# Optimization experiments

Hardware: AMD Instinct MI355X
Metric: run time of the kernel (lower is better)

The kernel has to match this reference:

```python
import jax, jax.numpy as jnp
import numpy as np

N = 50000      # occupied sparse voxels
C_IN = 512     # inplanes (= 4*planes for residual)
P = 128        # planes
K = 27         # 3x3x3 kernel volume in 3D
EPS = 1e-5
NEG = 0.1      # leaky-relu slope


def setup_inputs() -> dict:
    key = jax.random.key(0)
    k1, k2, k3, k4, k5, k6 = jax.random.split(key, 6)
    x = jax.random.normal(k1, (N, C_IN), dtype=jnp.float32)
    mask = (jax.random.uniform(k2, (N, 1)) > 0.3).astype(jnp.float32)
    nbr = jax.random.randint(k3, (N, K), 0, N, dtype=jnp.int32)
    W1 = jax.random.normal(k4, (C_IN, P), dtype=jnp.float32) * (1.0 / np.sqrt(C_IN))
    W2 = jax.random.normal(k5, (K, P, P), dtype=jnp.float32) * (1.0 / np.sqrt(K * P))
    W3 = jax.random.normal(k6, (P, C_IN), dtype=jnp.float32) * (1.0 / np.sqrt(P))
    return {"x": x, "mask": mask, "nbr": nbr, "W1": W1, "W2": W2, "W3": W3}


def lrelu(x):
    return jnp.where(x >= 0, x, NEG * x)


def inorm(x):
    # Minkowski instance norm: per-channel over all points of the instance
    mu = jnp.mean(x, axis=0, keepdims=True)
    var = jnp.var(x, axis=0, keepdims=True)
    return (x - mu) * jax.lax.rsqrt(var + EPS)


def pconv_k1(x, m, W):
    # 1x1x1 partial conv: mask, matmul, renormalize by coverage (=m itself)
    valid = (m > 0).astype(x.dtype)          # [N,1]
    return (x @ W) * valid, valid


def pconv_k3(x, m, nbr, W):
    # gather-GEMM partial conv over 27-neighborhood map
    mg = m[nbr]                                # [N,K,1]
    xg = x[nbr] * mg                           # [N,K,P] masked gather
    out = jnp.einsum('nkc,kcd->nd', xg, W)     # [N,P]
    msum = jnp.sum(mg, axis=1)                 # [N,1] coverage count
    ratio = (K / jnp.maximum(msum, 1.0)) * (msum > 0).astype(x.dtype)
    return out * ratio, (msum > 0).astype(x.dtype)


def reference(x, mask, nbr, W1, W2, W3):
    out, m = pconv_k1(x, mask, W1)
    out = lrelu(inorm(out))
    out, m = pconv_k3(out, m, nbr, W2)
    out = lrelu(inorm(out))
    out, m = pconv_k1(out, m, W3)
    out = inorm(out)
    out = lrelu(out + x)                       # residual (no downsample)
    m = jnp.clip(m + mask, 0.0, 1.0)           # mask residual + clamp
    return out, m
```

## Files before the change

### kernel.cpp

```cpp
#include <hip/hip_runtime.h>
#include <hip/hip_bf16.h>

#define NPTS 50000
#define CIN  512
#define PCH  128
#define KNB  27
#define EPSV 1e-5f
#define NEGS 0.1f

typedef __bf16 bf16;
typedef __bf16 bf16x8 __attribute__((ext_vector_type(8)));
typedef __bf16 bf16x4 __attribute__((ext_vector_type(4)));
typedef float  f32x4  __attribute__((ext_vector_type(4)));

typedef void __attribute__((address_space(3)))* as3ptr;
typedef const void __attribute__((address_space(1)))* as1ptr;
__device__ __forceinline__ void gl_lds16(const void* g, void* l) {
  __builtin_amdgcn_global_load_lds((as1ptr)g, (as3ptr)l, 16, 0, 0);
}


__global__ void xcvt_kernel(const float* __restrict__ x, bf16* __restrict__ xb) {
  int i = (blockIdx.x * blockDim.x + threadIdx.x) * 8;
  if (i >= NPTS * CIN) return;
  float4 a = *(const float4*)&x[i];
  float4 b = *(const float4*)&x[i + 4];
  bf16x8 o;
  o[0] = (bf16)a.x; o[1] = (bf16)a.y; o[2] = (bf16)a.z; o[3] = (bf16)a.w;
  o[4] = (bf16)b.x; o[5] = (bf16)b.y; o[6] = (bf16)b.z; o[7] = (bf16)b.w;
  *(bf16x8*)&xb[i] = o;
}

__global__ void tcvt_kernel(const float* __restrict__ src, bf16* __restrict__ dst,
                            int R, int Ccols) {
  int i = blockIdx.x * blockDim.x + threadIdx.x;
  if (i >= R * Ccols) return;
  int c = i / R, r = i - c * R;
  dst[i] = (bf16)src[(size_t)r * Ccols + c];
}

__global__ void tcvt_w2k_kernel(const float* __restrict__ src, bf16* __restrict__ dst) {
  int i = blockIdx.x * blockDim.x + threadIdx.x;
  if (i >= KNB * PCH * PCH) return;
  int k = i >> 14, rem = i & 16383;
  int d = rem >> 7, c = rem & 127;
  dst[i] = (bf16)src[(k << 14) + c * 128 + d];
}

__global__ void prep_kernel(const int* __restrict__ nbr, const float* __restrict__ mask,
                            int* __restrict__ nbrT, float* __restrict__ ratio,
                            float* __restrict__ valid2) {
  int n = blockIdx.x * blockDim.x + threadIdx.x;
  if (n >= NPTS) return;
  float s = 0.f;
#pragma unroll
  for (int k = 0; k < KNB; ++k) {
    int idx = nbr[n * KNB + k];
    nbrT[k * NPTS + n] = idx;
    s += (mask[idx] > 0.f) ? 1.f : 0.f;
  }
  ratio[n]  = s > 0.f ? 27.0f / s : 0.f;
  valid2[n] = s > 0.f ? 1.f : 0.f;
}

__global__ void finalize_kernel(const float* __restrict__ ssum, const float* __restrict__ ssq,
                                float* __restrict__ mu, float* __restrict__ inv) {
  int c = threadIdx.x;
  float m = ssum[c] / (float)NPTS;
  float v = ssq[c] / (float)NPTS - m * m;
  mu[c]  = m;
  inv[c] = rsqrtf(v + EPSV);
}

__global__ void ew_kernel(const float* __restrict__ in, const float* __restrict__ mu,
                          const float* __restrict__ inv, const float* __restrict__ rowmask,
                          bf16* __restrict__ outb) {
  int i = (blockIdx.x * blockDim.x + threadIdx.x) * 4;
  if (i >= NPTS * PCH) return;
  float4 v = *(const float4*)&in[i];
  int c = i & 127;
  int row = i >> 7;
  float mk = rowmask[row];
  float t0 = (v.x - mu[c + 0]) * inv[c + 0];
  float t1 = (v.y - mu[c + 1]) * inv[c + 1];
  float t2 = (v.z - mu[c + 2]) * inv[c + 2];
  float t3 = (v.w - mu[c + 3]) * inv[c + 3];
  t0 = (t0 >= 0.f ? t0 : NEGS * t0) * mk;
  t1 = (t1 >= 0.f ? t1 : NEGS * t1) * mk;
  t2 = (t2 >= 0.f ? t2 : NEGS * t2) * mk;
  t3 = (t3 >= 0.f ? t3 : NEGS * t3) * mk;
  bf16x4 o;
  o[0] = (bf16)t0; o[1] = (bf16)t1; o[2] = (bf16)t2; o[3] = (bf16)t3;
  *(bf16x4*)&outb[i] = o;
}

__global__ void final_kernel(const float* __restrict__ x, const bf16* __restrict__ out3n,
                             const float* __restrict__ mu, const float* __restrict__ inv,
                             float* __restrict__ out) {
  int i = (blockIdx.x * blockDim.x + threadIdx.x) * 8;
  if (i >= NPTS * CIN) return;
  bf16x8 v = *(const bf16x8*)&out3n[i];
  float4 x0 = *(const float4*)&x[i];
  float4 x1 = *(const float4*)&x[i + 4];
  int c = i & 511;
  float t[8];
  float xv[8] = {x0.x, x0.y, x0.z, x0.w, x1.x, x1.y, x1.z, x1.w};
#pragma unroll
  for (int q = 0; q < 8; ++q) {
    float u = ((float)v[q] - mu[c + q]) * inv[c + q] + xv[q];
    t[q] = u >= 0.f ? u : NEGS * u;
  }
  float4 o0 = {t[0], t[1], t[2], t[3]}, o1 = {t[4], t[5], t[6], t[7]};
  *(float4*)&out[i] = o0;
  *(float4*)&out[i + 4] = o1;
}

__global__ void maskout_kernel(const float* __restrict__ mask, const float* __restrict__ valid2,
                               float* __restrict__ outm) {
  int n = blockIdx.x * blockDim.x + threadIdx.x;
  if (n >= NPTS) return;
  outm[n] = fminf(valid2[n] + mask[n], 1.f);
}


__global__ __launch_bounds__(256) void gemm1_kernel(
    const bf16* __restrict__ xb, const bf16* __restrict__ w1t,
    const float* __restrict__ mask, float* __restrict__ out1,
    float* __restrict__ ssum, float* __restrict__ ssq) {
  __shared__ __align__(16) bf16 As[2][128 * 128];
  int row0 = blockIdx.x * 128;
  int tid = threadIdx.x;
  int lane = tid & 63, wid = tid >> 6;
  int mq = (wid >> 1) * 64, nq = (wid & 1) * 64;
  int lr = lane & 15, lq = lane >> 4;
  int rb = tid >> 4;
  int msw = (tid & 15) ^ (rb & 7);
  int rowc[8];
#pragma unroll
  for (int j = 0; j < 8; ++j) {
    int rr = row0 + rb + 16 * j;
    rowc[j] = rr < NPTS ? rr : NPTS - 1;
  }
  f32x4 acc[4][4];
#pragma unroll
  for (int i = 0; i < 4; ++i)
#pragma unroll
    for (int j = 0; j < 4; ++j)
#pragma unroll
      for (int r = 0; r < 4; ++r) acc[i][j][r] = 0.f;

#pragma unroll
  for (int j = 0; j < 8; ++j)
    gl_lds16(xb + (size_t)rowc[j] * CIN + (msw << 3),
             &As[0][(j * 256 + wid * 64) * 8]);
  __syncthreads();

  for (int kc = 0; kc < 4; ++kc) {
    int cur = kc & 1;
    if (kc < 3) {
#pragma unroll
      for (int j = 0; j < 8; ++j)
        gl_lds16(xb + (size_t)rowc[j] * CIN + (kc + 1) * 128 + (msw << 3),
                 &As[cur ^ 1][(j * 256 + wid * 64) * 8]);
    }
    const bf16* bp = w1t + (size_t)(nq + lr) * CIN + kc * 128 + lq * 8;
#pragma unroll
    for (int c0 = 0; c0 < 128; c0 += 32) {
      int cs = ((c0 >> 3) + lq) ^ (lr & 7);
      bf16x8 af[4], bfg[4];
#pragma unroll
      for (int i = 0; i < 4; ++i) af[i]  = *(const bf16x8*)&As[cur][(mq + i * 16 + lr) * 128 + cs * 8];
#pragma unroll
      for (int i = 0; i < 4; ++i) bfg[i] = *(const bf16x8*)(bp + (size_t)i * 16 * CIN + c0);
#pragma unroll
      for (int i = 0; i < 4; ++i)
#pragma unroll
        for (int j = 0; j < 4; ++j)
          acc[i][j] = __builtin_amdgcn_mfma_f32_16x16x32_bf16(af[i], bfg[j], acc[i][j], 0, 0, 0);
    }
    __syncthreads();
  }
  float rs[4][4];
#pragma unroll
  for (int i = 0; i < 4; ++i)
#pragma unroll
    for (int r = 0; r < 4; ++r) {
      int row = row0 + mq + i * 16 + lq * 4 + r;
      rs[i][r] = (row < NPTS) ? (mask[row] > 0.f ? 1.f : 0.f) : 0.f;
    }
#pragma unroll
  for (int j = 0; j < 4; ++j) {
    int col = nq + j * 16 + lr;
    float s = 0.f, q = 0.f;
#pragma unroll
    for (int i = 0; i < 4; ++i) {
#pragma unroll
      for (int r = 0; r < 4; ++r) {
        int row = row0 + mq + i * 16 + lq * 4 + r;
        if (row < NPTS) {
          float v = acc[i][j][r] * rs[i][r];
          out1[(size_t)row * PCH + col] = v;
          s += v; q += v * v;
        }
      }
    }
    s += __shfl_xor(s, 16); s += __shfl_xor(s, 32);
    q += __shfl_xor(q, 16); q += __shfl_xor(q, 32);
    if (lq == 0) { atomicAdd(&ssum[col], s); atomicAdd(&ssq[col], q); }
  }
}

__global__ __launch_bounds__(256) void gemm2_kernel(
    const bf16* __restrict__ a, const bf16* __restrict__ w2k,
    const int* __restrict__ nbrT, const float* __restrict__ ratio,
    float* __restrict__ out2, float* __restrict__ ssum, float* __restrict__ ssq) {
  __shared__ __align__(16) bf16 As[2][128 * 128];
  int row0 = blockIdx.x * 128;
  int tid = threadIdx.x;
  int lane = tid & 63, wid = tid >> 6;
  int mq = (wid >> 1) * 64, nq = (wid & 1) * 64;
  int lr = lane & 15, lq = lane >> 4;
  int rb = tid >> 4;
  int msw = (tid & 15) ^ (rb & 7);
  int rowc[8];
#pragma unroll
  for (int j = 0; j < 8; ++j) {
    int rr = row0 + rb + 16 * j;
    rowc[j] = rr < NPTS ? rr : NPTS - 1;
  }
  f32x4 acc[4][4];
#pragma unroll
  for (int i = 0; i < 4; ++i)
#pragma unroll
    for (int j = 0; j < 4; ++j)
#pragma unroll
      for (int r = 0; r < 4; ++r) acc[i][j][r] = 0.f;

  int nidx[8];
#pragma unroll
  for (int j = 0; j < 8; ++j) nidx[j] = nbrT[rowc[j]];
#pragma unroll
  for (int j = 0; j < 8; ++j)
    gl_lds16(a + (size_t)nidx[j] * PCH + (msw << 3),
             &As[0][(j * 256 + wid * 64) * 8]);
#pragma unroll
  for (int j = 0; j < 8; ++j) nidx[j] = nbrT[NPTS + rowc[j]];
  __syncthreads();

  for (int k = 0; k < KNB; ++k) {
    int cur = k & 1;
    if (k + 1 < KNB) {
#pragma unroll
      for (int j = 0; j < 8; ++j)
        gl_lds16(a + (size_t)nidx[j] * PCH + (msw << 3),
                 &As[cur ^ 1][(j * 256 + wid * 64) * 8]);
    }
    if (k + 2 < KNB) {
#pragma unroll
      for (int j = 0; j < 8; ++j) nidx[j] = nbrT[(k + 2) * NPTS + rowc[j]];
    }
    const bf16* bp = w2k + (size_t)k * PCH * PCH + (nq + lr) * PCH + lq * 8;
#pragma unroll
    for (int c0 = 0; c0 < 128; c0 += 32) {
      int cs = ((c0 >> 3) + lq) ^ (lr & 7);
      bf16x8 af[4], bfg[4];
#pragma unroll
      for (int i = 0; i < 4; ++i) af[i]  = *(const bf16x8*)&As[cur][(mq + i * 16 + lr) * 128 + cs * 8];
#pragma unroll
      for (int i = 0; i < 4; ++i) bfg[i] = *(const bf16x8*)(bp + (size_t)i * 16 * PCH + c0);
#pragma unroll
      for (int i = 0; i < 4; ++i)
#pragma unroll
        for (int j = 0; j < 4; ++j)
          acc[i][j] = __builtin_amdgcn_mfma_f32_16x16x32_bf16(af[i], bfg[j], acc[i][j], 0, 0, 0);
    }
    __syncthreads();
  }
  float rs[4][4];
#pragma unroll
  for (int i = 0; i < 4; ++i)
#pragma unroll
    for (int r = 0; r < 4; ++r) {
      int row = row0 + mq + i * 16 + lq * 4 + r;
      rs[i][r] = (row < NPTS) ? ratio[row] : 0.f;
    }
#pragma unroll
  for (int j = 0; j < 4; ++j) {
    int col = nq + j * 16 + lr;
    float s = 0.f, q = 0.f;
#pragma unroll
    for (int i = 0; i < 4; ++i) {
#pragma unroll
      for (int r = 0; r < 4; ++r) {
        int row = row0 + mq + i * 16 + lq * 4 + r;
        if (row < NPTS) {
          float v = acc[i][j][r] * rs[i][r];
          out2[(size_t)row * PCH + col] = v;
          s += v; q += v * v;
        }
      }
    }
    s += __shfl_xor(s, 16); s += __shfl_xor(s, 32);
    q += __shfl_xor(q, 16); q += __shfl_xor(q, 32);
    if (lq == 0) { atomicAdd(&ssum[col], s); atomicAdd(&ssq[col], q); }
  }
}

__global__ __launch_bounds__(256) void gemm3_kernel(
    const bf16* __restrict__ a, const bf16* __restrict__ w3t, bf16* __restrict__ out3n,
    float* __restrict__ ssum, float* __restrict__ ssq) {
  __shared__ __align__(16) bf16 As[128 * 128];
  int row0 = blockIdx.x * 128;
  int ncol0 = blockIdx.y * 128;
  int tid = threadIdx.x;
  int lane = tid & 63, wid = tid >> 6;
  int mq = (wid >> 1) * 64, nq = (wid & 1) * 64;
  int lr = lane & 15, lq = lane >> 4;
  int rb = tid >> 4;
  int msw = (tid & 15) ^ (rb & 7);
#pragma unroll
  for (int j = 0; j < 8; ++j) {
    int rr = row0 + rb + 16 * j;
    int rc = rr < NPTS ? rr : NPTS - 1;
    gl_lds16(a + (size_t)rc * PCH + (msw << 3),
             &As[(j * 256 + wid * 64) * 8]);
  }
  f32x4 acc[4][4];
#pragma unroll
  for (int i = 0; i < 4; ++i)
#pragma unroll
    for (int j = 0; j < 4; ++j)
#pragma unroll
      for (int r = 0; r < 4; ++r) acc[i][j][r] = 0.f;
  __syncthreads();
  const bf16* bp = w3t + (size_t)(ncol0 + nq + lr) * PCH + lq * 8;
#pragma unroll
  for (int c0 = 0; c0 < 128; c0 += 32) {
    int cs = ((c0 >> 3) + lq) ^ (lr & 7);
    bf16x8 af[4], bfg[4];
#pragma unroll
    for (int i = 0; i < 4; ++i) af[i]  = *(const bf16x8*)&As[(mq + i * 16 + lr) * 128 + cs * 8];
#pragma unroll
    for (int i = 0; i < 4; ++i) bfg[i] = *(const bf16x8*)(bp + (size_t)i * 16 * PCH + c0);
#pragma unroll
    for (int i = 0; i < 4; ++i)
#pragma unroll
      for (int j = 0; j < 4; ++j)
        acc[i][j] = __builtin_amdgcn_mfma_f32_16x16x32_bf16(af[i], bfg[j], acc[i][j], 0, 0, 0);
  }
#pragma unroll
  for (int j = 0; j < 4; ++j) {
    int col = ncol0 + nq + j * 16 + lr;
    float s = 0.f, q = 0.f;
#pragma unroll
    for (int i = 0; i < 4; ++i) {
#pragma unroll
      for (int r = 0; r < 4; ++r) {
        int row = row0 + mq + i * 16 + lq * 4 + r;
        if (row < NPTS) {
          float v = acc[i][j][r];
          out3n[(size_t)row * CIN + col] = (bf16)v;
          s += v; q += v * v;
        }
      }
    }
    s += __shfl_xor(s, 16); s += __shfl_xor(s, 32);
    q += __shfl_xor(q, 16); q += __shfl_xor(q, 32);
    if (lq == 0) { atomicAdd(&ssum[col], s); atomicAdd(&ssq[col], q); }
  }
}

extern "C" void kernel_launch(void* const* d_in, const int* in_sizes, int n_in,
                              void* d_out, int out_size, void* d_ws, size_t ws_size,
                              hipStream_t stream) {
  const float* x    = (const float*)d_in[0];
  const float* mask = (const float*)d_in[1];
  const int*   nbr  = (const int*)d_in[2];
  const float* W1   = (const float*)d_in[3];
  const float* W2   = (const float*)d_in[4];
  const float* W3   = (const float*)d_in[5];
  float* out = (float*)d_out;
  char* ws = (char*)d_ws;

  auto al = [](size_t x_) { return (x_ + 255) & ~(size_t)255; };
  size_t off = 0;
  size_t OFF_OUT1  = off; off += al((size_t)NPTS * PCH * 4);
  size_t OFF_OUT2  = off; off += al((size_t)NPTS * PCH * 4);
  size_t OFF_OUT1N = off; off += al((size_t)NPTS * PCH * 2);
  size_t OFF_OUT2N = off; off += al((size_t)NPTS * PCH * 2);
  size_t OFF_W1T   = off; off += al((size_t)PCH * CIN * 2);
  size_t OFF_W2K   = off; off += al((size_t)KNB * PCH * PCH * 2);
  size_t OFF_W3T   = off; off += al((size_t)CIN * PCH * 2);
  size_t OFF_NBRT  = off; off += al((size_t)KNB * NPTS * 4);
  size_t OFF_RATIO = off; off += al((size_t)NPTS * 4);
  size_t OFF_VAL2  = off; off += al((size_t)NPTS * 4);
  size_t OFF_SUMS  = off; off += al((size_t)1536 * 4);
  size_t OFF_PRMS  = off; off += al((size_t)1536 * 4);

  float* out1   = (float*)(ws + OFF_OUT1);
  float* out2   = (float*)(ws + OFF_OUT2);
  bf16*  out3n  = (bf16*)(ws + OFF_OUT1);
  bf16*  xb     = (bf16*)(ws + OFF_OUT2);
  bf16*  out1n  = (bf16*)(ws + OFF_OUT1N);
  bf16*  out2n  = (bf16*)(ws + OFF_OUT2N);
  bf16*  w1t    = (bf16*)(ws + OFF_W1T);
  bf16*  w2k    = (bf16*)(ws + OFF_W2K);
  bf16*  w3t    = (bf16*)(ws + OFF_W3T);
  int*   nbrT   = (int*)(ws + OFF_NBRT);
  float* ratio  = (float*)(ws + OFF_RATIO);
  float* valid2 = (float*)(ws + OFF_VAL2);
  float* sums   = (float*)(ws + OFF_SUMS);
  float* s1sum = sums, *s1sq = sums + 128;
  float* s2sum = sums + 256, *s2sq = sums + 384;
  float* s3sum = sums + 512, *s3sq = sums + 1024;
  float* prms = (float*)(ws + OFF_PRMS);
  float* mu1 = prms, *inv1 = prms + 128;
  float* mu2 = prms + 256, *inv2 = prms + 384;
  float* mu3 = prms + 512, *inv3 = prms + 1024;

  hipMemsetAsync(sums, 0, 1536 * 4, stream);

  prep_kernel<<<(NPTS + 255) / 256, 256, 0, stream>>>(nbr, mask, nbrT, ratio, valid2);
  tcvt_kernel<<<(CIN * PCH + 255) / 256, 256, 0, stream>>>(W1, w1t, CIN, PCH);
  tcvt_w2k_kernel<<<(KNB * PCH * PCH + 255) / 256, 256, 0, stream>>>(W2, w2k);
  tcvt_kernel<<<(PCH * CIN + 255) / 256, 256, 0, stream>>>(W3, w3t, PCH, CIN);
  xcvt_kernel<<<(NPTS * CIN / 8 + 255) / 256, 256, 0, stream>>>(x, xb);

  int mblocks = (NPTS + 127) / 128;

  gemm1_kernel<<<mblocks, 256, 0, stream>>>(xb, w1t, mask, out1, s1sum, s1sq);
  finalize_kernel<<<1, 128, 0, stream>>>(s1sum, s1sq, mu1, inv1);
  ew_kernel<<<(NPTS * PCH / 4 + 255) / 256, 256, 0, stream>>>(out1, mu1, inv1, mask, out1n);

  gemm2_kernel<<<mblocks, 256, 0, stream>>>(out1n, w2k, nbrT, ratio, out2, s2sum, s2sq);
  finalize_kernel<<<1, 128, 0, stream>>>(s2sum, s2sq, mu2, inv2);
  ew_kernel<<<(NPTS * PCH / 4 + 255) / 256, 256, 0, stream>>>(out2, mu2, inv2, valid2, out2n);

  dim3 g3(mblocks, 4);
  gemm3_kernel<<<g3, 256, 0, stream>>>(out2n, w3t, out3n, s3sum, s3sq);
  finalize_kernel<<<1, 512, 0, stream>>>(s3sum, s3sq, mu3, inv3);
  final_kernel<<<(NPTS * CIN / 8 + 255) / 256, 256, 0, stream>>>(x, out3n, mu3, inv3, out);
  maskout_kernel<<<(NPTS + 255) / 256, 256, 0, stream>>>(mask, valid2, out + (size_t)NPTS * CIN);
}
```

Baseline: 505.7 us.

## Merge prep kernels, fold mask output into final, retile GEMM warps, loop gemm3 columns

Five preprocessing launches (x conversion, three weight transposes, neighbor prep) become one preproc kernel, and the mask-output kernel is folded into the final elementwise kernel, cutting launch overhead. All three GEMMs change warp tiling from 64x64 per warp to 128 rows x 32 columns per warp, so each warp reads every A row from LDS and fewer B fragments per step. gemm3 now loops over four 128-column chunks inside one block, reusing the staged A tile instead of launching a 4-wide grid. This lowers parallelism for gemm3 and increases LDS reads of A per warp.

```diff
diff --git a/kernel.cpp b/kernel.cpp
--- a/kernel.cpp
+++ b/kernel.cpp
@@ -20,47 +20,61 @@
 }
 
 
-__global__ void xcvt_kernel(const float* __restrict__ x, bf16* __restrict__ xb) {
-  int i = (blockIdx.x * blockDim.x + threadIdx.x) * 8;
-  if (i >= NPTS * CIN) return;
-  float4 a = *(const float4*)&x[i];
-  float4 b = *(const float4*)&x[i + 4];
-  bf16x8 o;
-  o[0] = (bf16)a.x; o[1] = (bf16)a.y; o[2] = (bf16)a.z; o[3] = (bf16)a.w;
-  o[4] = (bf16)b.x; o[5] = (bf16)b.y; o[6] = (bf16)b.z; o[7] = (bf16)b.w;
-  *(bf16x8*)&xb[i] = o;
-}
-
-__global__ void tcvt_kernel(const float* __restrict__ src, bf16* __restrict__ dst,
-                            int R, int Ccols) {
+__global__ void preproc_kernel(const float* __restrict__ x, const float* __restrict__ mask,
+                               const int* __restrict__ nbr,
+                               const float* __restrict__ W1, const float* __restrict__ W2,
+                               const float* __restrict__ W3,
+                               bf16* __restrict__ xb, int* __restrict__ nbrT,
+                               float* __restrict__ ratio, float* __restrict__ valid2,
+                               bf16* __restrict__ w1t, bf16* __restrict__ w2k,
+                               bf16* __restrict__ w3t) {
   int i = blockIdx.x * blockDim.x + threadIdx.x;
-  if (i >= R * Ccols) return;
-  int c = i / R, r = i - c * R;
-  dst[i] = (bf16)src[(size_t)r * Ccols + c];
-}
-
-__global__ void tcvt_w2k_kernel(const float* __restrict__ src, bf16* __restrict__ dst) {
-  int i = blockIdx.x * blockDim.x + threadIdx.x;
-  if (i >= KNB * PCH * PCH) return;
-  int k = i >> 14, rem = i & 16383;
-  int d = rem >> 7, c = rem & 127;
-  dst[i] = (bf16)src[(k << 14) + c * 128 + d];
-}
-
-__global__ void prep_kernel(const int* __restrict__ nbr, const float* __restrict__ mask,
-                            int* __restrict__ nbrT, float* __restrict__ ratio,
-                            float* __restrict__ valid2) {
-  int n = blockIdx.x * blockDim.x + threadIdx.x;
-  if (n >= NPTS) return;
-  float s = 0.f;
-#pragma unroll
-  for (int k = 0; k < KNB; ++k) {
-    int idx = nbr[n * KNB + k];
-    nbrT[k * NPTS + n] = idx;
-    s += (mask[idx] > 0.f) ? 1.f : 0.f;
-  }
-  ratio[n]  = s > 0.f ? 27.0f / s : 0.f;
-  valid2[n] = s > 0.f ? 1.f : 0.f;
+  const int NX = NPTS * CIN / 8;
+  if (i < NX) {
+    int e = i * 8;
+    float4 a = *(const float4*)&x[e];
+    float4 b = *(const float4*)&x[e + 4];
+    bf16x8 o;
+    o[0] = (bf16)a.x; o[1] = (bf16)a.y; o[2] = (bf16)a.z; o[3] = (bf16)a.w;
+    o[4] = (bf16)b.x; o[5] = (bf16)b.y; o[6] = (bf16)b.z; o[7] = (bf16)b.w;
+    *(bf16x8*)&xb[e] = o;
+    return;
+  }
+  i -= NX;
+  const int NW2 = KNB * PCH * PCH;
+  if (i < NW2) {
+    int k = i >> 14, rem = i & 16383;
+    int d = rem >> 7, c = rem & 127;
+    w2k[i] = (bf16)W2[(k << 14) + c * 128 + d];
+    return;
+  }
+  i -= NW2;
+  const int NW1 = CIN * PCH;
+  if (i < NW1) {
+    int c = i / CIN, r = i - c * CIN;
+    w1t[i] = (bf16)W1[r * PCH + c];
+    return;
+  }
+  i -= NW1;
+  const int NW3 = PCH * CIN;
+  if (i < NW3) {
+    int c = i / PCH, r = i - c * PCH;
+    w3t[i] = (bf16)W3[r * CIN + c];
+    return;
+  }
+  i -= NW3;
+  if (i < NPTS) {
+    int n = i;
+    float s = 0.f;
+#pragma unroll
+    for (int k = 0; k < KNB; ++k) {
+      int idx = nbr[n * KNB + k];
+      nbrT[k * NPTS + n] = idx;
+      s += (mask[idx] > 0.f) ? 1.f : 0.f;
+    }
+    ratio[n]  = s > 0.f ? 27.0f / s : 0.f;
+    valid2[n] = s > 0.f ? 1.f : 0.f;
+  }
 }
 
 __global__ void finalize_kernel(const float* __restrict__ ssum, const float* __restrict__ ssq,
@@ -96,8 +110,13 @@
 
 __global__ void final_kernel(const float* __restrict__ x, const bf16* __restrict__ out3n,
                              const float* __restrict__ mu, const float* __restrict__ inv,
+                             const float* __restrict__ mask, const float* __restrict__ valid2,
                              float* __restrict__ out) {
-  int i = (blockIdx.x * blockDim.x + threadIdx.x) * 8;
+  int gid = blockIdx.x * blockDim.x + threadIdx.x;
+  if (gid < NPTS) {
+    out[(size_t)NPTS * CIN + gid] = fminf(valid2[gid] + mask[gid], 1.f);
+  }
+  int i = gid * 8;
   if (i >= NPTS * CIN) return;
   bf16x8 v = *(const bf16x8*)&out3n[i];
   float4 x0 = *(const float4*)&x[i];
@@ -113,13 +132,6 @@
   float4 o0 = {t[0], t[1], t[2], t[3]}, o1 = {t[4], t[5], t[6], t[7]};
   *(float4*)&out[i] = o0;
   *(float4*)&out[i + 4] = o1;
-}
-
-__global__ void maskout_kernel(const float* __restrict__ mask, const float* __restrict__ valid2,
-                               float* __restrict__ outm) {
-  int n = blockIdx.x * blockDim.x + threadIdx.x;
-  if (n >= NPTS) return;
-  outm[n] = fminf(valid2[n] + mask[n], 1.f);
 }
 
 
@@ -131,7 +143,7 @@
   int row0 = blockIdx.x * 128;
   int tid = threadIdx.x;
   int lane = tid & 63, wid = tid >> 6;
-  int mq = (wid >> 1) * 64, nq = (wid & 1) * 64;
+  int nq = wid * 32;
   int lr = lane & 15, lq = lane >> 4;
   int rb = tid >> 4;
   int msw = (tid & 15) ^ (rb & 7);
@@ -141,11 +153,11 @@
     int rr = row0 + rb + 16 * j;
     rowc[j] = rr < NPTS ? rr : NPTS - 1;
   }
-  f32x4 acc[4][4];
-#pragma unroll
-  for (int i = 0; i < 4; ++i)
-#pragma unroll
-    for (int j = 0; j < 4; ++j)
+  f32x4 acc[8][2];
+#pragma unroll
+  for (int i = 0; i < 8; ++i)
+#pragma unroll
+    for (int j = 0; j < 2; ++j)
 #pragma unroll
       for (int r = 0; r < 4; ++r) acc[i][j][r] = 0.f;
 
@@ -165,38 +177,38 @@
     }
     const bf16* bp = w1t + (size_t)(nq + lr) * CIN + kc * 128 + lq * 8;
 #pragma unroll
-    for (int c0 = 0; c0 < 128; c0 += 32) {
-      int cs = ((c0 >> 3) + lq) ^ (lr & 7);
-      bf16x8 af[4], bfg[4];
-#pragma unroll
-      for (int i = 0; i < 4; ++i) af[i]  = *(const bf16x8*)&As[cur][(mq + i * 16 + lr) * 128 + cs * 8];
-#pragma unroll
-      for (int i = 0; i < 4; ++i) bfg[i] = *(const bf16x8*)(bp + (size_t)i * 16 * CIN + c0);
-#pragma unroll
-      for (int i = 0; i < 4; ++i)
-#pragma unroll
-        for (int j = 0; j < 4; ++j)
+    for (int c0i = 0; c0i < 4; ++c0i) {
+      int cs = ((c0i << 2) + lq) ^ (lr & 7);
+      bf16x8 af[8], bfg[2];
+#pragma unroll
+      for (int i = 0; i < 8; ++i) af[i] = *(const bf16x8*)&As[cur][(i * 16 + lr) * 128 + cs * 8];
+#pragma unroll
+      for (int j = 0; j < 2; ++j) bfg[j] = *(const bf16x8*)(bp + (size_t)j * 16 * CIN + c0i * 32);
+#pragma unroll
+      for (int i = 0; i < 8; ++i)
+#pragma unroll
+        for (int j = 0; j < 2; ++j)
           acc[i][j] = __builtin_amdgcn_mfma_f32_16x16x32_bf16(af[i], bfg[j], acc[i][j], 0, 0, 0);
     }
     __syncthreads();
   }
-  float rs[4][4];
-#pragma unroll
-  for (int i = 0; i < 4; ++i)
+  float rs[8][4];
+#pragma unroll
+  for (int i = 0; i < 8; ++i)
 #pragma unroll
     for (int r = 0; r < 4; ++r) {
-      int row = row0 + mq + i * 16 + lq * 4 + r;
+      int row = row0 + i * 16 + lq * 4 + r;
       rs[i][r] = (row < NPTS) ? (mask[row] > 0.f ? 1.f : 0.f) : 0.f;
     }
 #pragma unroll
-  for (int j = 0; j < 4; ++j) {
+  for (int j = 0; j < 2; ++j) {
     int col = nq + j * 16 + lr;
     float s = 0.f, q = 0.f;
 #pragma unroll
-    for (int i = 0; i < 4; ++i) {
+    for (int i = 0; i < 8; ++i) {
 #pragma unroll
       for (int r = 0; r < 4; ++r) {
-        int row = row0 + mq + i * 16 + lq * 4 + r;
+        int row = row0 + i * 16 + lq * 4 + r;
         if (row < NPTS) {
           float v = acc[i][j][r] * rs[i][r];
           out1[(size_t)row * PCH + col] = v;
@@ -218,7 +230,7 @@
   int row0 = blockIdx.x * 128;
   int tid = threadIdx.x;
   int lane = tid & 63, wid = tid >> 6;
-  int mq = (wid >> 1) * 64, nq = (wid & 1) * 64;
+  int nq = wid * 32;
   int lr = lane & 15, lq = lane >> 4;
   int rb = tid >> 4;
   int msw = (tid & 15) ^ (rb & 7);
@@ -228,11 +240,11 @@
     int rr = row0 + rb + 16 * j;
     rowc[j] = rr < NPTS ? rr : NPTS - 1;
   }
-  f32x4 acc[4][4];
-#pragma unroll
-  for (int i = 0; i < 4; ++i)
-#pragma unroll
-    for (int j = 0; j < 4; ++j)
+  f32x4 acc[8][2];
+#pragma unroll
+  for (int i = 0; i < 8; ++i)
+#pragma unroll
+    for (int j = 0; j < 2; ++j)
 #pragma unroll
       for (int r = 0; r < 4; ++r) acc[i][j][r] = 0.f;
 
@@ -259,40 +271,40 @@
 #pragma unroll
       for (int j = 0; j < 8; ++j) nidx[j] = nbrT[(k + 2) * NPTS + rowc[j]];
     }
-    const bf16* bp = w2k + (size_t)k * PCH * PCH + (nq + lr) * PCH + lq * 8;
-#pragma unroll
-    for (int c0 = 0; c0 < 128; c0 += 32) {
-      int cs = ((c0 >> 3) + lq) ^ (lr & 7);
-      bf16x8 af[4], bfg[4];
-#pragma unroll
-      for (int i = 0; i < 4; ++i) af[i]  = *(const bf16x8*)&As[cur][(mq + i * 16 + lr) * 128 + cs * 8];
-#pragma unroll
-      for (int i = 0; i < 4; ++i) bfg[i] = *(const bf16x8*)(bp + (size_t)i * 16 * PCH + c0);
-#pragma unroll
-      for (int i = 0; i < 4; ++i)
-#pragma unroll
-        for (int j = 0; j < 4; ++j)
+    const bf16* bp = w2k + ((size_t)k << 14) + (nq + lr) * PCH + lq * 8;
+#pragma unroll
+    for (int c0i = 0; c0i < 4; ++c0i) {
+      int cs = ((c0i << 2) + lq) ^ (lr & 7);
+      bf16x8 af[8], bfg[2];
+#pragma unroll
+      for (int i = 0; i < 8; ++i) af[i] = *(const bf16x8*)&As[cur][(i * 16 + lr) * 128 + cs * 8];
+#pragma unroll
+      for (int j = 0; j < 2; ++j) bfg[j] = *(const bf16x8*)(bp + (size_t)j * 16 * PCH + c0i * 32);
+#pragma unroll
+      for (int i = 0; i < 8; ++i)
+#pragma unroll
+        for (int j = 0; j < 2; ++j)
           acc[i][j] = __builtin_amdgcn_mfma_f32_16x16x32_bf16(af[i], bfg[j], acc[i][j], 0, 0, 0);
     }
     __syncthreads();
   }
-  float rs[4][4];
-#pragma unroll
-  for (int i = 0; i < 4; ++i)
+  float rs[8][4];
+#pragma unroll
+  for (int i = 0; i < 8; ++i)
 #pragma unroll
     for (int r = 0; r < 4; ++r) {
-      int row = row0 + mq + i * 16 + lq * 4 + r;
+      int row = row0 + i * 16 + lq * 4 + r;
       rs[i][r] = (row < NPTS) ? ratio[row] : 0.f;
     }
 #pragma unroll
-  for (int j = 0; j < 4; ++j) {
+  for (int j = 0; j < 2; ++j) {
     int col = nq + j * 16 + lr;
     float s = 0.f, q = 0.f;
 #pragma unroll
-    for (int i = 0; i < 4; ++i) {
+    for (int i = 0; i < 8; ++i) {
 #pragma unroll
       for (int r = 0; r < 4; ++r) {
-        int row = row0 + mq + i * 16 + lq * 4 + r;
+        int row = row0 + i * 16 + lq * 4 + r;
         if (row < NPTS) {
           float v = acc[i][j][r] * rs[i][r];
           out2[(size_t)row * PCH + col] = v;
@@ -311,10 +323,9 @@
     float* __restrict__ ssum, float* __restrict__ ssq) {
   __shared__ __align__(16) bf16 As[128 * 128];
   int row0 = blockIdx.x * 128;
-  int ncol0 = blockIdx.y * 128;
   int tid = threadIdx.x;
   int lane = tid & 63, wid = tid >> 6;
-  int mq = (wid >> 1) * 64, nq = (wid & 1) * 64;
+  int nq = wid * 32;
   int lr = lane & 15, lq = lane >> 4;
   int rb = tid >> 4;
   int msw = (tid & 15) ^ (rb & 7);
@@ -325,48 +336,52 @@
     gl_lds16(a + (size_t)rc * PCH + (msw << 3),
              &As[(j * 256 + wid * 64) * 8]);
   }
-  f32x4 acc[4][4];
-#pragma unroll
-  for (int i = 0; i < 4; ++i)
-#pragma unroll
-    for (int j = 0; j < 4; ++j)
-#pragma unroll
-      for (int r = 0; r < 4; ++r) acc[i][j][r] = 0.f;
   __syncthreads();
-  const bf16* bp = w3t + (size_t)(ncol0 + nq + lr) * PCH + lq * 8;
-#pragma unroll
-  for (int c0 = 0; c0 < 128; c0 += 32) {
-    int cs = ((c0 >> 3) + lq) ^ (lr & 7);
-    bf16x8 af[4], bfg[4];
-#pragma unroll
-    for (int i = 0; i < 4; ++i) af[i]  = *(const bf16x8*)&As[(mq + i * 16 + lr) * 128 + cs * 8];
-#pragma unroll
-    for (int i = 0; i < 4; ++i) bfg[i] = *(const bf16x8*)(bp + (size_t)i * 16 * PCH + c0);
-#pragma unroll
-    for (int i = 0; i < 4; ++i)
-#pragma unroll
-      for (int j = 0; j < 4; ++j)
-        acc[i][j] = __builtin_amdgcn_mfma_f32_16x16x32_bf16(af[i], bfg[j], acc[i][j], 0, 0, 0);
-  }
-#pragma unroll
-  for (int j = 0; j < 4; ++j) {
-    int col = ncol0 + nq + j * 16 + lr;
-    float s = 0.f, q = 0.f;
-#pragma unroll
-    for (int i = 0; i < 4; ++i) {
-#pragma unroll
-      for (int r = 0; r < 4; ++r) {
-        int row = row0 + mq + i * 16 + lq * 4 + r;
-        if (row < NPTS) {
-          float v = acc[i][j][r];
-          out3n[(size_t)row * CIN + col] = (bf16)v;
-          s += v; q += v * v;
+
+  for (int yc = 0; yc < 4; ++yc) {
+    int ncol0 = yc * 128;
+    const bf16* bp = w3t + (size_t)(ncol0 + nq + lr) * PCH + lq * 8;
+    f32x4 acc[8][2];
+#pragma unroll
+    for (int i = 0; i < 8; ++i)
+#pragma unroll
+      for (int j = 0; j < 2; ++j)
+#pragma unroll
+        for (int r = 0; r < 4; ++r) acc[i][j][r] = 0.f;
+#pragma unroll
+    for (int c0i = 0; c0i < 4; ++c0i) {
+      int cs = ((c0i << 2) + lq) ^ (lr & 7);
+      bf16x8 af[8], bfg[2];
+#pragma unroll
+      for (int i = 0; i < 8; ++i) af[i] = *(const bf16x8*)&As[(i * 16 + lr) * 128 + cs * 8];
+#pragma unroll
+      for (int j = 0; j < 2; ++j) bfg[j] = *(const bf16x8*)(bp + (size_t)j * 16 * PCH + c0i * 32);
+#pragma unroll
+      for (int i = 0; i < 8; ++i)
+#pragma unroll
+        for (int j = 0; j < 2; ++j)
+          acc[i][j] = __builtin_amdgcn_mfma_f32_16x16x32_bf16(af[i], bfg[j], acc[i][j], 0, 0, 0);
+    }
+#pragma unroll
+    for (int j = 0; j < 2; ++j) {
+      int col = ncol0 + nq + j * 16 + lr;
+      float s = 0.f, q = 0.f;
+#pragma unroll
+      for (int i = 0; i < 8; ++i) {
+#pragma unroll
+        for (int r = 0; r < 4; ++r) {
+          int row = row0 + i * 16 + lq * 4 + r;
+          if (row < NPTS) {
+            float v = acc[i][j][r];
+            out3n[(size_t)row * CIN + col] = (bf16)v;
+            s += v; q += v * v;
+          }
         }
       }
-    }
-    s += __shfl_xor(s, 16); s += __shfl_xor(s, 32);
-    q += __shfl_xor(q, 16); q += __shfl_xor(q, 32);
-    if (lq == 0) { atomicAdd(&ssum[col], s); atomicAdd(&ssq[col], q); }
+      s += __shfl_xor(s, 16); s += __shfl_xor(s, 32);
+      q += __shfl_xor(q, 16); q += __shfl_xor(q, 32);
+      if (lq == 0) { atomicAdd(&ssum[col], s); atomicAdd(&ssq[col], q); }
+    }
   }
 }
 
@@ -420,11 +435,9 @@
 
   hipMemsetAsync(sums, 0, 1536 * 4, stream);
 
-  prep_kernel<<<(NPTS + 255) / 256, 256, 0, stream>>>(nbr, mask, nbrT, ratio, valid2);
-  tcvt_kernel<<<(CIN * PCH + 255) / 256, 256, 0, stream>>>(W1, w1t, CIN, PCH);
-  tcvt_w2k_kernel<<<(KNB * PCH * PCH + 255) / 256, 256, 0, stream>>>(W2, w2k);
-  tcvt_kernel<<<(PCH * CIN + 255) / 256, 256, 0, stream>>>(W3, w3t, PCH, CIN);
-  xcvt_kernel<<<(NPTS * CIN / 8 + 255) / 256, 256, 0, stream>>>(x, xb);
+  const int NPRE = NPTS * CIN / 8 + KNB * PCH * PCH + CIN * PCH + PCH * CIN + NPTS;
+  preproc_kernel<<<(NPRE + 255) / 256, 256, 0, stream>>>(
+      x, mask, nbr, W1, W2, W3, xb, nbrT, ratio, valid2, w1t, w2k, w3t);
 
   int mblocks = (NPTS + 127) / 128;
 
@@ -436,9 +449,8 @@
   finalize_kernel<<<1, 128, 0, stream>>>(s2sum, s2sq, mu2, inv2);
   ew_kernel<<<(NPTS * PCH / 4 + 255) / 256, 256, 0, stream>>>(out2, mu2, inv2, valid2, out2n);
 
-  dim3 g3(mblocks, 4);
-  gemm3_kernel<<<g3, 256, 0, stream>>>(out2n, w3t, out3n, s3sum, s3sq);
+  gemm3_kernel<<<mblocks, 256, 0, stream>>>(out2n, w3t, out3n, s3sum, s3sq);
   finalize_kernel<<<1, 512, 0, stream>>>(s3sum, s3sq, mu3, inv3);
-  final_kernel<<<(NPTS * CIN / 8 + 255) / 256, 256, 0, stream>>>(x, out3n, mu3, inv3, out);
-  maskout_kernel<<<(NPTS + 255) / 256, 256, 0, stream>>>(mask, valid2, out + (size_t)NPTS * CIN);
-}
+  final_kernel<<<(NPTS * CIN / 8 + 255) / 256, 256, 0, stream>>>(
+      x, out3n, mu3, inv3, mask, valid2, out);
+}
```

Measured after the change: 423.2 us. 1.19x faster.
